# Kernel optimization log

Measured on AMD Instinct MI355X. Metric: run time of the kernel, lower is better.

The kernel has to match this reference:

```python
import jax, jax.numpy as jnp
import numpy as np

B, T, C = 2, 2048, 2048
H = 16
HS = C // H           # 128
ROT = HS // 2         # 64 partial-rotary dims
BASE = 10000.0


def setup_inputs() -> dict:
    key = jax.random.key(0)
    ks = jax.random.split(key, 9)
    s = 1.0 / np.sqrt(C)
    return {
        "x": jax.random.normal(ks[0], (B, T, C), jnp.float32),
        "Wq": jax.random.normal(ks[1], (C, C), jnp.float32) * s,
        "bq": jax.random.normal(ks[2], (C,), jnp.float32) * 0.02,
        "Wk": jax.random.normal(ks[3], (C, C), jnp.float32) * s,
        "bk": jax.random.normal(ks[4], (C,), jnp.float32) * 0.02,
        "Wv": jax.random.normal(ks[5], (C, C), jnp.float32) * s,
        "bv": jax.random.normal(ks[6], (C,), jnp.float32) * 0.02,
        "Wo": jax.random.normal(ks[7], (C, C), jnp.float32) * s,
        "bo": jax.random.normal(ks[8], (C,), jnp.float32) * 0.02,
    }


def _rotate_half(u):
    u1, u2 = u[..., : u.shape[-1] // 2], u[..., u.shape[-1] // 2 :]
    return jnp.concatenate((-u2, u1), axis=-1)


def _rope_tables(t_len):
    inv_freq = 1.0 / (BASE ** (jnp.arange(0, ROT, 2, dtype=jnp.float32) / ROT))
    freqs = jnp.arange(t_len, dtype=jnp.float32)[:, None] * inv_freq[None, :]
    emb = jnp.concatenate((freqs, freqs), axis=-1)  # [T, ROT]
    return jnp.cos(emb), jnp.sin(emb)


def reference(x, Wq, bq, Wk, bk, Wv, bv, Wo, bo):
    Bs, Ts, Cs = x.shape
    q = (x @ Wq.T + bq).reshape(Bs, Ts, H, HS).transpose(0, 2, 1, 3)  # [B,H,T,HS]
    k = (x @ Wk.T + bk).reshape(Bs, Ts, H, HS).transpose(0, 2, 1, 3)
    v = (x @ Wv.T + bv).reshape(Bs, Ts, H, HS).transpose(0, 2, 1, 3)

    # partial rotary on first ROT dims of each head
    cos, sin = _rope_tables(Ts)  # [T, ROT] broadcast over B,H
    q_rot, q_pass = q[..., :ROT], q[..., ROT:]
    k_rot, k_pass = k[..., :ROT], k[..., ROT:]
    q_rot = q_rot * cos + _rotate_half(q_rot) * sin
    k_rot = k_rot * cos + _rotate_half(k_rot) * sin
    q = jnp.concatenate((q_rot, q_pass), axis=-1)
    k = jnp.concatenate((k_rot, k_pass), axis=-1)

    att = jnp.einsum("bhqd,bhkd->bhqk", q, k) * (1.0 / np.sqrt(HS))
    causal = jnp.tril(jnp.ones((Ts, Ts), dtype=bool))
    att = jnp.where(causal, att, jnp.float32(-jnp.inf))
    att = jax.nn.softmax(att, axis=-1)
    out = jnp.einsum("bhqk,bhkd->bhqd", att, v)          # [B,H,T,HS]
    out = out.transpose(0, 2, 1, 3).reshape(Bs, Ts, Cs)  # [B,T,C]
    return out @ Wo.T + bo
```

## Files before the change

### kernel.cpp

```cpp
#include <hip/hip_runtime.h>
#include <hip/hip_bf16.h>

#define Bdim 2
#define Tdim 2048
#define Cdim 2048
#define Hn   16

using bf16x8 = __attribute__((ext_vector_type(8))) short;
using f32x4  = __attribute__((ext_vector_type(4))) float;
using f32x16 = __attribute__((ext_vector_type(16))) float;
typedef __hip_bfloat16 bf16;

#define VMWAIT(n) asm volatile("s_waitcnt vmcnt(" #n ")" ::: "memory")
#define CROW(r, hi) (((r) & 3) + 8 * ((r) >> 2) + 4 * (hi))
#define QS2 ((float)(0.08838834764831845 * 1.4426950408889634))
#define THR2 11.5415603f

__device__ __forceinline__ void load_lds16(const void* g, void* l) {
  __builtin_amdgcn_global_load_lds(
      (const __attribute__((address_space(1))) void*)g,
      (__attribute__((address_space(3))) void*)l, 16, 0, 0);
}

__device__ __forceinline__ float bf2f(unsigned short u) {
  union { unsigned int i; float f; } x; x.i = ((unsigned int)u) << 16; return x.f;
}
__device__ __forceinline__ unsigned short f2bf(float f) {
  bf16 h = __float2bfloat16(f); return *(unsigned short*)&h;
}
__device__ __forceinline__ unsigned cvtpk(float lo, float hi) {
  unsigned r;
  asm volatile("v_cvt_pk_bf16_f32 %0, %1, %2" : "=v"(r) : "v"(lo), "v"(hi));
  return r;
}

__global__ __launch_bounds__(256) void cvt_all(const float* __restrict__ x,
                                               const float* __restrict__ w0,
                                               const float* __restrict__ w1,
                                               const float* __restrict__ w2,
                                               const float* __restrict__ w3,
                                               bf16* __restrict__ dx,
                                               bf16* __restrict__ d0,
                                               bf16* __restrict__ d1,
                                               bf16* __restrict__ d2,
                                               bf16* __restrict__ d3) {
  const int NX = (Bdim * Tdim * Cdim) / 4;
  const int NW = (Cdim * Cdim) / 4;
  int i = blockIdx.x * 256 + threadIdx.x;
  int stride = gridDim.x * 256;
  for (; i < NX + 4 * NW; i += stride) {
    const float* s; bf16* d; int j;
    if (i < NX) { s = x; d = dx; j = i; }
    else {
      int k = i - NX;
      int wsel = k >> 20;
      j = k & (NW - 1);
      s = wsel == 0 ? w0 : wsel == 1 ? w1 : wsel == 2 ? w2 : w3;
      d = wsel == 0 ? d0 : wsel == 1 ? d1 : wsel == 2 ? d2 : d3;
    }
    float4 v = ((const float4*)s)[j];
    ushort4 o;
    o.x = f2bf(v.x); o.y = f2bf(v.y); o.z = f2bf(v.z); o.w = f2bf(v.w);
    ((ushort4*)d)[j] = o;
  }
}

__global__ __launch_bounds__(256) void rope_tables_k(float2* __restrict__ cst) {
  int idx = blockIdx.x * blockDim.x + threadIdx.x;
  if (idx >= Tdim * 32) return;
  int t = idx >> 5, i = idx & 31;
  double f = pow(10000.0, -(double)i / 32.0);
  double ang = (double)t * f;
  cst[idx] = make_float2((float)cos(ang), (float)sin(ang));
}

__global__ __launch_bounds__(512, 2) void gemmQKV(
    const bf16* __restrict__ A, const bf16* __restrict__ Wcat,
    const float* __restrict__ b0, const float* __restrict__ b1, const float* __restrict__ b2,
    bf16* __restrict__ oq, bf16* __restrict__ ok, bf16* __restrict__ vt,
    const float2* __restrict__ cst) {
  extern __shared__ char lds[];
  const int K = 2048;
  const int tid = threadIdx.x, lane = tid & 63, wid = tid >> 6;
  const int l15 = lane & 15, lhi = lane >> 4;
  const int wr = wid >> 2, wc = wid & 3;

  const int q8 = gridDim.x >> 3;
  const int swz = ((int)blockIdx.x & 7) * q8 + ((int)blockIdx.x >> 3);
  const int bm = (swz >> 4) * 128;
  const int strip = swz & 15;

  const int rA = tid >> 3;
  const int sl = tid & 7;
  const bf16* thrA = A + (size_t)(bm + rA) * K + ((sl ^ (rA & 7)) << 3);
  const int colB = strip * 384 + ((rA >> 5) * 96) + (rA & 31);
  const bf16* thrB = Wcat + (size_t)colB * K + ((sl ^ (rA & 7)) << 3);
  const int wbase = wid * 1024;

#define BUF(T) (lds + (((T) & 1) ? 65536 : 0))
#define SAU(T, U) load_lds16(thrA + (size_t)(U) * 64 * 2048 + (T) * 64, \
                             BUF(T) + (U) * 8192 + wbase)
#define SBU(T, NT, U) load_lds16(thrB + (size_t)((NT) * 32 + (U) * 192) * 2048 + (T) * 64, \
                                 BUF(T) + 16384 + (NT) * 16384 + (U) * 8192 + wbase)

  f32x4 acc[4][6] = {};
  const int NT = 32;
  const int asw = (l15 & 7) << 4;
  bf16x8 afr[4][2], bfr[2][2];

#define READA(T)                                                                 \
  _Pragma("unroll")                                                              \
  for (int mi = 0; mi < 4; ++mi)                                                 \
    _Pragma("unroll")                                                            \
    for (int kk = 0; kk < 2; ++kk)                                               \
      afr[mi][kk] = *(const bf16x8*)(BUF(T) + (wr * 64 + mi * 16 + l15) * 128    \
                                     + ((kk * 64 + lhi * 16) ^ asw));

#define READB(T, NT_)                                                            \
  _Pragma("unroll")                                                              \
  for (int j = 0; j < 2; ++j)                                                    \
    _Pragma("unroll")                                                            \
    for (int kk = 0; kk < 2; ++kk)                                               \
      bfr[j][kk] = *(const bf16x8*)(BUF(T) + 16384 + (NT_) * 16384               \
                                    + (wc * 32 + j * 16 + l15) * 128             \
                                    + ((kk * 64 + lhi * 16) ^ asw));

#define MF(NT_)                                                                  \
  __builtin_amdgcn_s_setprio(1);                                                 \
  _Pragma("unroll")                                                              \
  for (int mi = 0; mi < 4; ++mi)                                                 \
    _Pragma("unroll")                                                            \
    for (int j = 0; j < 2; ++j)                                                  \
      _Pragma("unroll")                                                          \
      for (int kk = 0; kk < 2; ++kk)                                             \
        acc[mi][(NT_) * 2 + j] = __builtin_amdgcn_mfma_f32_16x16x32_bf16(        \
            afr[mi][kk], bfr[j][kk], acc[mi][(NT_) * 2 + j], 0, 0, 0);           \
  __builtin_amdgcn_s_setprio(0);

#define BARS()                                                                   \
  __builtin_amdgcn_s_barrier();                                                  \
  asm volatile("s_waitcnt lgkmcnt(0)" ::: "memory");                             \
  __builtin_amdgcn_sched_barrier(0);

#define BARE() __builtin_amdgcn_s_barrier();

  SAU(0, 0); SAU(0, 1);
  SBU(0, 0, 0); SBU(0, 0, 1);
  SBU(0, 1, 0); SBU(0, 1, 1);
  SBU(0, 2, 0); SBU(0, 2, 1);
  SAU(1, 0); SAU(1, 1);
  SBU(1, 0, 0); SBU(1, 0, 1);
  SBU(1, 1, 0); SBU(1, 1, 1);
  VMWAIT(6);
  __builtin_amdgcn_s_barrier();

  for (int t = 0; t < NT - 2; ++t) {
    READA(t); READB(t, 0);
    SBU(t + 1, 2, 0); SBU(t + 1, 2, 1);
    BARS(); MF(0); BARE();
    READB(t, 1);
    SAU(t + 2, 0); SAU(t + 2, 1);
    SBU(t + 2, 0, 0); SBU(t + 2, 0, 1);
    BARS(); MF(1); BARE();
    READB(t, 2);
    SBU(t + 2, 1, 0); SBU(t + 2, 1, 1);
    VMWAIT(6);
    BARS(); MF(2); BARE();
  }
  {
    const int t = NT - 2;
    READA(t); READB(t, 0);
    SBU(t + 1, 2, 0); SBU(t + 1, 2, 1);
    BARS(); MF(0); BARE();
    READB(t, 1);
    BARS(); MF(1); BARE();
    READB(t, 2);
    VMWAIT(0);
    BARS(); MF(2); BARE();
  }
  {
    const int t = NT - 1;
    READA(t); READB(t, 0);
    BARS(); MF(0); BARE();
    READB(t, 1);
    BARS(); MF(1); BARE();
    READB(t, 2);
    BARS(); MF(2); BARE();
  }

  __syncthreads();
  if (wc == 3) {
    #pragma unroll
    for (int mi = 0; mi < 4; ++mi)
      #pragma unroll
      for (int j = 0; j < 2; ++j) {
        const int col = strip * 384 + 288 + j * 16 + l15;
        const int mat = col >> 11;
        const float bv = (mat == 0 ? b0 : mat == 1 ? b1 : b2)[col & 2047];
        f32x4 v = acc[mi][j];
        v[0] += bv; v[1] += bv; v[2] += bv; v[3] += bv;
        *(f32x4*)(lds + ((((wr * 4 + mi) * 2 + j) * 4 + lhi) * 16 + l15) * 16) = v;
      }
  }
  __syncthreads();

  #pragma unroll
  for (int mi = 0; mi < 4; ++mi) {
    const int row = bm + wr * 64 + mi * 16 + lhi * 4;
    const int bb = row >> 11, tt = row & 2047;
    #pragma unroll
    for (int nt = 0; nt < 3; ++nt)
      #pragma unroll
      for (int j = 0; j < 2; ++j) {
        const int col = strip * 384 + wc * 96 + nt * 32 + j * 16 + l15;
        const int mat = col >> 11;
        const int ocol = col & 2047;
        const float bv = (mat == 0 ? b0 : mat == 1 ? b1 : b2)[ocol];
        if (mat == 2) {
          const int hh = ocol >> 7, dd = ocol & 127;
          ushort4 pk;
          pk.x = f2bf(acc[mi][nt * 2 + j][0] + bv);
          pk.y = f2bf(acc[mi][nt * 2 + j][1] + bv);
          pk.z = f2bf(acc[mi][nt * 2 + j][2] + bv);
          pk.w = f2bf(acc[mi][nt * 2 + j][3] + bv);
          *(ushort4*)(vt + ((size_t)((bb * 16 + hh) * 128 + dd)) * 2048 + tt) = pk;
        } else {
          const float qs = (mat == 0) ? QS2 : 1.0f;
          bf16* obf = (mat == 0) ? oq : ok;
          int cat;
          if (wc == 0)      cat = (nt == 0) ? 1 : (nt == 1) ? 2 : 0;
          else if (wc == 1) cat = (nt == 1) ? 1 : (nt == 2) ? 2 : 0;
          else if (wc == 2) cat = (nt == 2) ? 3 : 0;
          else              cat = (nt == 0) ? 2 : 0;
          if (cat == 0) {
            #pragma unroll
            for (int r = 0; r < 4; ++r)
              obf[(size_t)(row + r) * 2048 + ocol] =
                  __float2bfloat16((acc[mi][nt * 2 + j][r] + bv) * qs);
          } else if (cat == 1) {
            const float bv1 = (mat == 0 ? b0 : b1)[ocol + 32];
            const int d = j * 16 + l15;
            #pragma unroll
            for (int r = 0; r < 4; ++r) {
              float2 cs = cst[(tt + r) * 32 + d];
              float u0 = acc[mi][nt * 2 + j][r] + bv;
              float u1 = acc[mi][(nt + 1) * 2 + j][r] + bv1;
              obf[(size_t)(row + r) * 2048 + ocol] =
                  __float2bfloat16((u0 * cs.x - u1 * cs.y) * qs);
              obf[(size_t)(row + r) * 2048 + ocol + 32] =
                  __float2bfloat16((u1 * cs.x + u0 * cs.y) * qs);
            }
          } else if (cat == 3) {
            f32x4 ux = *(const f32x4*)(lds + ((((wr * 4 + mi) * 2 + j) * 4 + lhi) * 16 + l15) * 16);
            const int d = j * 16 + l15;
            #pragma unroll
            for (int r = 0; r < 4; ++r) {
              float2 cs = cst[(tt + r) * 32 + d];
              float u0 = acc[mi][4 + j][r] + bv;
              float u1 = ux[r];
              obf[(size_t)(row + r) * 2048 + ocol] =
                  __float2bfloat16((u0 * cs.x - u1 * cs.y) * qs);
              obf[(size_t)(row + r) * 2048 + ocol + 32] =
                  __float2bfloat16((u1 * cs.x + u0 * cs.y) * qs);
            }
          }
        }
      }
  }
#undef BUF
#undef SAU
#undef SBU
#undef READA
#undef READB
#undef MF
#undef BARS
#undef BARE
}

__global__ __launch_bounds__(512, 2) void gemmWo(
    const bf16* __restrict__ A, const bf16* __restrict__ W0,
    const float* __restrict__ b0, float* __restrict__ out, int K, int nby) {
  extern __shared__ char lds[];
  const int tid = threadIdx.x, lane = tid & 63, wid = tid >> 6;
  const int l15 = lane & 15, lhi = lane >> 4;
  const int wr = wid >> 2, wc = wid & 3;
  const int fb = (wc & 1) | ((wc >> 1) << 2);

  const int q8 = gridDim.x >> 3;
  const int swz = ((int)blockIdx.x & 7) * q8 + ((int)blockIdx.x >> 3);
  const int bm = (swz / nby) * 128, bn = (swz % nby) * 256;
  const bf16* Asrc = A + (size_t)bm * K;
  const bf16* Wsrc = W0 + (size_t)bn * K;

  const bf16 *sA0, *sA1, *sB00, *sB01, *sB10, *sB11;
  {
    int c = tid, r = c >> 3, sl = c & 7;
    size_t off = (size_t)r * K + ((sl ^ (r & 7)) << 3);
    sA0 = Asrc + off;
    sA1 = Asrc + (size_t)64 * K + off;
    sB00 = Wsrc + off;
    sB10 = Wsrc + (size_t)128 * K + off;
  }
  {
    int c = 512 + tid, r = c >> 3, sl = c & 7;
    size_t off = (size_t)r * K + ((sl ^ (r & 7)) << 3);
    sB01 = Wsrc + off;
    sB11 = Wsrc + (size_t)128 * K + off;
  }
  const int ldsA = wid * 1024;

#define SA0(t) load_lds16(sA0 + (t) * 64, lds + ((t) & 1) * 49152 + ldsA)
#define SA1(t) load_lds16(sA1 + (t) * 64, lds + ((t) & 1) * 49152 + 8192 + ldsA)
#define SB0(t) { load_lds16(sB00 + (t) * 64, lds + ((t) & 1) * 49152 + 16384 + ldsA); \
                 load_lds16(sB01 + (t) * 64, lds + ((t) & 1) * 49152 + 24576 + ldsA); }
#define SB1(t) { load_lds16(sB10 + (t) * 64, lds + ((t) & 1) * 49152 + 32768 + ldsA); \
                 load_lds16(sB11 + (t) * 64, lds + ((t) & 1) * 49152 + 40960 + ldsA); }

  f32x4 acc[4][4] = {};
  const int NT = K / 64;
  const int NI = NT / 2;
  const int asw = (l15 & 7) << 4;
  bf16x8 afr[2][2], bfr0[2][2], bfr1[2][2];

#define READ_A(BASE)                                                            \
  _Pragma("unroll")                                                             \
  for (int ii = 0; ii < 2; ++ii)                                                \
    _Pragma("unroll")                                                           \
    for (int kk = 0; kk < 2; ++kk)                                              \
      afr[ii][kk] = *(const bf16x8*)((BASE) + (wr * 32 + ii * 16 + l15) * 128   \
                                     + ((kk * 64 + lhi * 16) ^ asw));

#define READ_B(BASE, DST)                                                       \
  _Pragma("unroll")                                                             \
  for (int j = 0; j < 2; ++j)                                                   \
    _Pragma("unroll")                                                           \
    for (int kk = 0; kk < 2; ++kk)                                              \
      DST[j][kk] = *(const bf16x8*)((BASE) + ((fb + 2 * j) * 16 + l15) * 128    \
                                    + ((kk * 64 + lhi * 16) ^ asw));

#define MFMA_Q(MH, NH, BF)                                                      \
  __builtin_amdgcn_s_setprio(1);                                                \
  _Pragma("unroll")                                                             \
  for (int ii = 0; ii < 2; ++ii)                                                \
    _Pragma("unroll")                                                           \
    for (int j = 0; j < 2; ++j)                                                 \
      _Pragma("unroll")                                                         \
      for (int kk = 0; kk < 2; ++kk)                                            \
        acc[(MH) * 2 + ii][(NH) * 2 + j] =                                      \
            __builtin_amdgcn_mfma_f32_16x16x32_bf16(                            \
                afr[ii][kk], BF[j][kk], acc[(MH) * 2 + ii][(NH) * 2 + j], 0, 0, 0); \
  __builtin_amdgcn_s_setprio(0);

#define BAR_IN()                                                                \
  __builtin_amdgcn_s_barrier();                                                 \
  asm volatile("s_waitcnt lgkmcnt(0)" ::: "memory");                            \
  __builtin_amdgcn_sched_barrier(0);

#define BAR_OUT() __builtin_amdgcn_s_barrier();

  SA0(0); SB0(0); SB1(0); SA1(0);
  SA0(1); SB0(1); SB1(1);
  VMWAIT(5);
  __builtin_amdgcn_s_barrier();

  char* const buf0 = lds;
  char* const buf1 = lds + 49152;

  for (int i = 0; i < NI; ++i) {
    const int t0 = 2 * i, t1 = t0 + 1;
    const bool lastI = (i == NI - 1);

    READ_A(buf0);
    READ_B(buf0 + 16384, bfr0);
    SA1(t1);
    BAR_IN(); MFMA_Q(0, 0, bfr0); BAR_OUT();

    READ_B(buf0 + 32768, bfr1);
    if (!lastI) SA0(t0 + 2);
    BAR_IN(); MFMA_Q(0, 1, bfr1); BAR_OUT();

    READ_A(buf0 + 8192);
    if (!lastI) SB0(t0 + 2);
    BAR_IN(); MFMA_Q(1, 0, bfr0); BAR_OUT();

    if (!lastI) { SB1(t0 + 2); VMWAIT(5); } else VMWAIT(0);
    BAR_IN(); MFMA_Q(1, 1, bfr1); BAR_OUT();

    READ_A(buf1);
    READ_B(buf1 + 16384, bfr0);
    if (!lastI) SA1(t0 + 2);
    BAR_IN(); MFMA_Q(0, 0, bfr0); BAR_OUT();

    READ_B(buf1 + 32768, bfr1);
    if (!lastI) SA0(t1 + 2);
    BAR_IN(); MFMA_Q(0, 1, bfr1); BAR_OUT();

    READ_A(buf1 + 8192);
    if (!lastI) SB0(t1 + 2);
    BAR_IN(); MFMA_Q(1, 0, bfr0); BAR_OUT();

    if (!lastI) { SB1(t1 + 2); VMWAIT(5); }
    BAR_IN(); MFMA_Q(1, 1, bfr1); BAR_OUT();
  }

  #pragma unroll
  for (int mi = 0; mi < 4; ++mi) {
    const int row = bm + (mi >> 1) * 64 + wr * 32 + (mi & 1) * 16 + lhi * 4;
    #pragma unroll
    for (int nj = 0; nj < 4; ++nj) {
      const int col = bn + (nj >> 1) * 128 + (fb + 2 * (nj & 1)) * 16 + l15;
      const float bv = b0[col];
      #pragma unroll
      for (int r = 0; r < 4; ++r)
        out[(size_t)(row + r) * 2048 + col] = acc[mi][nj][r] + bv;
    }
  }
#undef SA0
#undef SA1
#undef SB0
#undef SB1
#undef READ_A
#undef READ_B
#undef MFMA_Q
#undef BAR_IN
#undef BAR_OUT
}

__global__ __launch_bounds__(256, 2) void attn_kernel(const bf16* __restrict__ Q,
                                                      const bf16* __restrict__ Kb,
                                                      const bf16* __restrict__ Vt,
                                                      bf16* __restrict__ O) {
  extern __shared__ char lds[];
  const int tid = threadIdx.x, lane = tid & 63, wave = tid >> 6;
  const int l31 = lane & 31, hi = lane >> 5;
  const int hi16 = hi << 4;

  const int bid = blockIdx.x;
  const int half = bid >> 8;
  const int idx = bid & 255;
  const int g = idx >> 5;
  const int qt = half ? g : (15 - g);
  const int bh = idx & 31;
  const int b = bh >> 4, h = bh & 15;
  const size_t bT = (size_t)b * Tdim;

  const int qb = qt * 128 + wave * 32;
  const int myq = qb + l31;

  bf16x8 qf[8];
  {
    const bf16* qrow = Q + (bT + myq) * Cdim + h * 128;
    #pragma unroll
    for (int ds = 0; ds < 8; ++ds)
      qf[ds] = *(const bf16x8*)(qrow + ds * 16 + hi * 8);
  }

  auto stageKV = [&](int kt) {
    const int k0 = kt * 64;
    char* kb = lds + (kt & 1) * 16384;
    char* vb = lds + 32768 + (kt & 1) * 16384;
    #pragma unroll
    for (int i = 0; i < 4; ++i) {
      int cb = i * 256 + wave * 64;
      int c = cb + lane;
      {
        int row = c >> 4, slot = c & 15;
        load_lds16(Kb + (bT + k0 + row) * Cdim + h * 128 + ((slot ^ (row & 7)) << 3),
                   kb + cb * 16);
      }
      {
        int row = c >> 3, slot = c & 7;
        load_lds16(Vt + ((size_t)(bh * 128 + row)) * Tdim + k0 + ((slot ^ (row & 7)) << 3),
                   vb + cb * 16);
      }
    }
  };

  f32x16 o[4] = {};
  float mrun = -1e30f, lrun = 0.f;

  const int nt = 2 * (qt + 1);
  stageKV(0);

  for (int kt = 0; kt < nt; ++kt) {
    if (kt + 1 < nt) { stageKV(kt + 1); VMWAIT(8); } else { VMWAIT(0); }
    __syncthreads();
    const char* kbuf = lds + (kt & 1) * 16384;
    const char* vbuf = lds + 32768 + (kt & 1) * 16384;
    const int k0 = kt * 64;

    const bool active = (k0 <= qb + 31);
    if (active) {
      f32x16 s0 = {}, s1 = {};
      const int krow0 = l31, krow1 = 32 + l31;
      const int ksw = (l31 & 7) << 4;
      __builtin_amdgcn_s_setprio(1);
      #pragma unroll
      for (int ds = 0; ds < 8; ++ds) {
        const int boff = (ds * 32 + hi16) ^ ksw;
        bf16x8 kf0 = *(const bf16x8*)(kbuf + krow0 * 256 + boff);
        bf16x8 kf1 = *(const bf16x8*)(kbuf + krow1 * 256 + boff);
        s0 = __builtin_amdgcn_mfma_f32_32x32x16_bf16(kf0, qf[ds], s0, 0, 0, 0);
        s1 = __builtin_amdgcn_mfma_f32_32x32x16_bf16(kf1, qf[ds], s1, 0, 0, 0);
      }
      __builtin_amdgcn_s_setprio(0);

      if (k0 + 63 > qb) {
        #pragma unroll
        for (int r = 0; r < 16; ++r) {
          const int key = k0 + CROW(r, hi);
          if (key > myq)      s0[r] = -1e30f;
          if (key + 32 > myq) s1[r] = -1e30f;
        }
      }

      float mx = s0[0];
      #pragma unroll
      for (int r = 1; r < 16; ++r) mx = fmaxf(mx, s0[r]);
      #pragma unroll
      for (int r = 0; r < 16; ++r) mx = fmaxf(mx, s1[r]);
      mx = fmaxf(mx, __shfl_xor(mx, 32));
      if (!__all(mx <= mrun + THR2)) {
        const float mnew = fmaxf(mrun, mx);
        const float scl = __builtin_amdgcn_exp2f(mrun - mnew);
        lrun *= scl;
        #pragma unroll
        for (int r = 0; r < 16; ++r) {
          const float sr = __shfl(scl, CROW(r, hi));
          o[0][r] *= sr; o[1][r] *= sr; o[2][r] *= sr; o[3][r] *= sr;
        }
        mrun = mnew;
      }
      float p0[16], p1[16];
      float ps = 0.f;
      #pragma unroll
      for (int r = 0; r < 16; ++r) {
        p0[r] = __builtin_amdgcn_exp2f(s0[r] - mrun); ps += p0[r];
        p1[r] = __builtin_amdgcn_exp2f(s1[r] - mrun); ps += p1[r];
      }
      ps += __shfl_xor(ps, 32);
      lrun += ps;

      unsigned u0[8], u1[8];
      #pragma unroll
      for (int gg = 0; gg < 4; ++gg) {
        u0[gg * 2 + 0] = cvtpk(p0[gg * 4 + 0], p0[gg * 4 + 1]);
        u0[gg * 2 + 1] = cvtpk(p0[gg * 4 + 2], p0[gg * 4 + 3]);
        u1[gg * 2 + 0] = cvtpk(p1[gg * 4 + 0], p1[gg * 4 + 1]);
        u1[gg * 2 + 1] = cvtpk(p1[gg * 4 + 2], p1[gg * 4 + 3]);
      }
      bf16x8 paf[4];
      #pragma unroll
      for (int s = 0; s < 2; ++s) {
        const unsigned* us = s ? u1 : u0;
        #pragma unroll
        for (int gp = 0; gp < 2; ++gp) {
          unsigned snd0 = hi ? us[4 * gp + 0] : us[4 * gp + 2];
          unsigned snd1 = hi ? us[4 * gp + 1] : us[4 * gp + 3];
          unsigned rcv0 = __shfl_xor((int)snd0, 32);
          unsigned rcv1 = __shfl_xor((int)snd1, 32);
          union { unsigned w[4]; bf16x8 v; } fr;
          if (hi == 0) {
            fr.w[0] = us[4 * gp + 0]; fr.w[1] = us[4 * gp + 1];
            fr.w[2] = rcv0;           fr.w[3] = rcv1;
          } else {
            fr.w[0] = rcv0;           fr.w[1] = rcv1;
            fr.w[2] = us[4 * gp + 2]; fr.w[3] = us[4 * gp + 3];
          }
          paf[s * 2 + gp] = fr.v;
        }
      }

      __builtin_amdgcn_s_setprio(1);
      #pragma unroll
      for (int dblk = 0; dblk < 4; ++dblk) {
        const int d = dblk * 32 + l31;
        const int vswz = (d & 7) << 4;
        #pragma unroll
        for (int ks = 0; ks < 4; ++ks) {
          bf16x8 vf = *(const bf16x8*)(vbuf + d * 128 + ((ks * 32 + hi16) ^ vswz));
          o[dblk] = __builtin_amdgcn_mfma_f32_32x32x16_bf16(paf[ks], vf, o[dblk], 0, 0, 0);
        }
      }
      __builtin_amdgcn_s_setprio(0);
    }
    __syncthreads();
  }

  const float inv = 1.f / lrun;
  #pragma unroll
  for (int r = 0; r < 16; ++r) {
    const float ir = __shfl(inv, CROW(r, hi));
    const int qrow = qb + CROW(r, hi);
    bf16* orow = O + (bT + qrow) * Cdim + h * 128;
    #pragma unroll
    for (int dblk = 0; dblk < 4; ++dblk)
      orow[dblk * 32 + l31] = __float2bfloat16(o[dblk][r] * ir);
  }
}

extern "C" void kernel_launch(void* const* d_in, const int* in_sizes, int n_in,
                              void* d_out, int out_size, void* d_ws, size_t ws_size,
                              hipStream_t stream) {
  const float* x  = (const float*)d_in[0];
  const float* Wq = (const float*)d_in[1];
  const float* bq = (const float*)d_in[2];
  const float* Wk = (const float*)d_in[3];
  const float* bk = (const float*)d_in[4];
  const float* Wv = (const float*)d_in[5];
  const float* bv = (const float*)d_in[6];
  const float* Wo = (const float*)d_in[7];
  const float* bo = (const float*)d_in[8];

  char* ws = (char*)d_ws;
  const size_t SZ_X  = (size_t)Bdim * Tdim * Cdim * 2;
  const size_t SZ_W  = (size_t)Cdim * Cdim * 2;
  bf16* x_bf  = (bf16*)(ws);
  bf16* Wq_bf = (bf16*)(ws + SZ_X);
  bf16* Wk_bf = (bf16*)(ws + SZ_X + SZ_W);
  bf16* Wv_bf = (bf16*)(ws + SZ_X + 2 * SZ_W);
  bf16* Wo_bf = (bf16*)(ws + SZ_X + 3 * SZ_W);
  bf16* q_bf  = (bf16*)(ws + SZ_X + 4 * SZ_W);
  bf16* k_bf  = (bf16*)(ws + 2 * SZ_X + 4 * SZ_W);
  bf16* v_t   = (bf16*)(ws + 3 * SZ_X + 4 * SZ_W);
  bf16* a_bf  = (bf16*)(ws + 4 * SZ_X + 4 * SZ_W);
  float2* cst = (float2*)(ws + 5 * SZ_X + 4 * SZ_W);

  const int K = Cdim;

  rope_tables_k<<<(Tdim * 32 + 255) / 256, 256, 0, stream>>>(cst);
  cvt_all<<<2048, 256, 0, stream>>>(x, Wq, Wk, Wv, Wo,
                                    x_bf, Wq_bf, Wk_bf, Wv_bf, Wo_bf);

  gemmQKV<<<512, 512, 131072, stream>>>(
      x_bf, Wq_bf, bq, bk, bv, q_bf, k_bf, v_t, cst);

  attn_kernel<<<512, 256, 65536, stream>>>(q_bf, k_bf, v_t, a_bf);

  gemmWo<<<256, 512, 98304, stream>>>(
      a_bf, Wo_bf, bo, (float*)d_out, K, 8);
}
```

Measured before the change: 236.3 us.

## Restructure QKV GEMM to 256x384 tiles with 32x32 MFMA and triple-buffered K=32 stages

The fused QKV projection kernel now uses 256-row by 384-column block tiles (256 blocks instead of 512) with 32x32x16 bf16 MFMA instructions in place of 16x16x32. Each K step is 32 wide, and three LDS stage buffers are rotated so global-to-LDS loads run two steps ahead. The epilogue is rewritten for the 32x32 accumulator layout and still applies RoPE, scaling and the V transpose. The aim is more data reuse per block and fewer LDS reads per MFMA. The cost is only 256 blocks, which may leave the grid with fewer waves than there are CUs to fill, and a reduced occupancy margin.

```diff
diff --git a/kernel.cpp b/kernel.cpp
--- a/kernel.cpp
+++ b/kernel.cpp
@@ -80,199 +80,195 @@
     bf16* __restrict__ oq, bf16* __restrict__ ok, bf16* __restrict__ vt,
     const float2* __restrict__ cst) {
   extern __shared__ char lds[];
-  const int K = 2048;
   const int tid = threadIdx.x, lane = tid & 63, wid = tid >> 6;
-  const int l15 = lane & 15, lhi = lane >> 4;
+  const int l31 = lane & 31, hi = lane >> 5;
   const int wr = wid >> 2, wc = wid & 3;
+  const int wbase = wid * 1024;
 
   const int q8 = gridDim.x >> 3;
   const int swz = ((int)blockIdx.x & 7) * q8 + ((int)blockIdx.x >> 3);
-  const int bm = (swz >> 4) * 128;
+  const int bm = (swz >> 4) * 256;
   const int strip = swz & 15;
 
-  const int rA = tid >> 3;
-  const int sl = tid & 7;
-  const bf16* thrA = A + (size_t)(bm + rA) * K + ((sl ^ (rA & 7)) << 3);
-  const int colB = strip * 384 + ((rA >> 5) * 96) + (rA & 31);
-  const bf16* thrB = Wcat + (size_t)colB * K + ((sl ^ (rA & 7)) << 3);
-  const int wbase = wid * 1024;
-
-#define BUF(T) (lds + (((T) & 1) ? 65536 : 0))
-#define SAU(T, U) load_lds16(thrA + (size_t)(U) * 64 * 2048 + (T) * 64, \
-                             BUF(T) + (U) * 8192 + wbase)
-#define SBU(T, NT, U) load_lds16(thrB + (size_t)((NT) * 32 + (U) * 192) * 2048 + (T) * 64, \
-                                 BUF(T) + 16384 + (NT) * 16384 + (U) * 8192 + wbase)
-
-  f32x4 acc[4][6] = {};
-  const int NT = 32;
-  const int asw = (l15 & 7) << 4;
-  bf16x8 afr[4][2], bfr[2][2];
-
-#define READA(T)                                                                 \
-  _Pragma("unroll")                                                              \
-  for (int mi = 0; mi < 4; ++mi)                                                 \
-    _Pragma("unroll")                                                            \
-    for (int kk = 0; kk < 2; ++kk)                                               \
-      afr[mi][kk] = *(const bf16x8*)(BUF(T) + (wr * 64 + mi * 16 + l15) * 128    \
-                                     + ((kk * 64 + lhi * 16) ^ asw));
-
-#define READB(T, NT_)                                                            \
-  _Pragma("unroll")                                                              \
-  for (int j = 0; j < 2; ++j)                                                    \
-    _Pragma("unroll")                                                            \
-    for (int kk = 0; kk < 2; ++kk)                                               \
-      bfr[j][kk] = *(const bf16x8*)(BUF(T) + 16384 + (NT_) * 16384               \
-                                    + (wc * 32 + j * 16 + l15) * 128             \
-                                    + ((kk * 64 + lhi * 16) ^ asw));
-
-#define MF(NT_)                                                                  \
-  __builtin_amdgcn_s_setprio(1);                                                 \
-  _Pragma("unroll")                                                              \
-  for (int mi = 0; mi < 4; ++mi)                                                 \
-    _Pragma("unroll")                                                            \
-    for (int j = 0; j < 2; ++j)                                                  \
-      _Pragma("unroll")                                                          \
-      for (int kk = 0; kk < 2; ++kk)                                             \
-        acc[mi][(NT_) * 2 + j] = __builtin_amdgcn_mfma_f32_16x16x32_bf16(        \
-            afr[mi][kk], bfr[j][kk], acc[mi][(NT_) * 2 + j], 0, 0, 0);           \
+  const int rS = tid >> 2, sS = tid & 3;
+  const int ssw = (sS ^ ((rS >> 1) & 3)) << 3;
+  const bf16* thrA = A + (size_t)(bm + rS) * 2048 + ssw;
+  const bf16* thrB = Wcat + (size_t)(strip * 384 + rS) * 2048 + ssw;
+
+#define SA(T, DB) { load_lds16(thrA + (T) * 32, (DB) + wbase);                              \
+                    load_lds16(thrA + (size_t)128 * 2048 + (T) * 32, (DB) + 8192 + wbase); }
+#define SB(T, DB) { load_lds16(thrB + (T) * 32, (DB) + 16384 + wbase);                      \
+                    load_lds16(thrB + (size_t)128 * 2048 + (T) * 32, (DB) + 24576 + wbase); \
+                    load_lds16(thrB + (size_t)256 * 2048 + (T) * 32, (DB) + 32768 + wbase); }
+
+  f32x16 acc[4][3] = {};
+  bf16x8 afr[4], bfr[3];
+  const int q2 = (l31 >> 1) & 3;
+  const int aoff = (wr * 128 + l31) * 64;
+  const int boff = 16384 + (wc * 96 + l31) * 64;
+  const int sl0 = (hi ^ q2) << 4;
+  const int sl1 = sl0 ^ 32;
+
+#define READF(PB, SL)                                                        \
+  {                                                                          \
+    const char* _p = (PB);                                                   \
+    _Pragma("unroll")                                                        \
+    for (int m_ = 0; m_ < 4; ++m_)                                           \
+      afr[m_] = *(const bf16x8*)(_p + aoff + m_ * 2048 + (SL));              \
+    _Pragma("unroll")                                                        \
+    for (int n_ = 0; n_ < 3; ++n_)                                           \
+      bfr[n_] = *(const bf16x8*)(_p + boff + n_ * 2048 + (SL));              \
+  }
+
+#define MF12()                                                               \
+  __builtin_amdgcn_s_setprio(1);                                             \
+  _Pragma("unroll")                                                          \
+  for (int m_ = 0; m_ < 4; ++m_)                                             \
+    _Pragma("unroll")                                                        \
+    for (int n_ = 0; n_ < 3; ++n_)                                           \
+      acc[m_][n_] = __builtin_amdgcn_mfma_f32_32x32x16_bf16(                 \
+          afr[m_], bfr[n_], acc[m_][n_], 0, 0, 0);                           \
   __builtin_amdgcn_s_setprio(0);
 
-#define BARS()                                                                   \
-  __builtin_amdgcn_s_barrier();                                                  \
-  asm volatile("s_waitcnt lgkmcnt(0)" ::: "memory");                             \
+#define BARS()                                                               \
+  __builtin_amdgcn_s_barrier();                                              \
+  asm volatile("s_waitcnt lgkmcnt(0)" ::: "memory");                         \
   __builtin_amdgcn_sched_barrier(0);
 
 #define BARE() __builtin_amdgcn_s_barrier();
 
-  SAU(0, 0); SAU(0, 1);
-  SBU(0, 0, 0); SBU(0, 0, 1);
-  SBU(0, 1, 0); SBU(0, 1, 1);
-  SBU(0, 2, 0); SBU(0, 2, 1);
-  SAU(1, 0); SAU(1, 1);
-  SBU(1, 0, 0); SBU(1, 0, 1);
-  SBU(1, 1, 0); SBU(1, 1, 1);
-  VMWAIT(6);
+  SA(0, lds); SB(0, lds);
+  SA(1, lds + 40960); SB(1, lds + 40960);
+  VMWAIT(5);
   __builtin_amdgcn_s_barrier();
 
+  const char* rb = lds;
+  char* sb = lds + 81920;
+  const int NT = 64;
+
   for (int t = 0; t < NT - 2; ++t) {
-    READA(t); READB(t, 0);
-    SBU(t + 1, 2, 0); SBU(t + 1, 2, 1);
-    BARS(); MF(0); BARE();
-    READB(t, 1);
-    SAU(t + 2, 0); SAU(t + 2, 1);
-    SBU(t + 2, 0, 0); SBU(t + 2, 0, 1);
-    BARS(); MF(1); BARE();
-    READB(t, 2);
-    SBU(t + 2, 1, 0); SBU(t + 2, 1, 1);
-    VMWAIT(6);
-    BARS(); MF(2); BARE();
+    READF(rb, sl0);
+    SA(t + 2, sb);
+    BARS(); MF12(); BARE();
+    READF(rb, sl1);
+    SB(t + 2, sb);
+    VMWAIT(5);
+    BARS(); MF12(); BARE();
+    rb = (rb == lds + 81920) ? lds : rb + 40960;
+    sb = (sb == lds + 81920) ? lds : sb + 40960;
   }
   {
-    const int t = NT - 2;
-    READA(t); READB(t, 0);
-    SBU(t + 1, 2, 0); SBU(t + 1, 2, 1);
-    BARS(); MF(0); BARE();
-    READB(t, 1);
-    BARS(); MF(1); BARE();
-    READB(t, 2);
+    READF(rb, sl0);
+    BARS(); MF12(); BARE();
+    READF(rb, sl1);
     VMWAIT(0);
-    BARS(); MF(2); BARE();
+    BARS(); MF12(); BARE();
+    rb = (rb == lds + 81920) ? lds : rb + 40960;
   }
   {
-    const int t = NT - 1;
-    READA(t); READB(t, 0);
-    BARS(); MF(0); BARE();
-    READB(t, 1);
-    BARS(); MF(1); BARE();
-    READB(t, 2);
-    BARS(); MF(2); BARE();
+    READF(rb, sl0);
+    BARS(); MF12(); BARE();
+    READF(rb, sl1);
+    BARS(); MF12(); BARE();
   }
 
   __syncthreads();
   if (wc == 3) {
+    const int col0 = strip * 384 + 288;
+    const int mat = col0 >> 11;
+    if (mat < 2) {
+      const int oc0 = col0 & 2047;
+      const float bv = (mat == 0 ? b0 : b1)[oc0 + l31];
+      #pragma unroll
+      for (int m = 0; m < 4; ++m)
+        #pragma unroll
+        for (int g = 0; g < 4; ++g) {
+          f32x4 v;
+          v[0] = acc[m][0][4 * g + 0] + bv;
+          v[1] = acc[m][0][4 * g + 1] + bv;
+          v[2] = acc[m][0][4 * g + 2] + bv;
+          v[3] = acc[m][0][4 * g + 3] + bv;
+          *(f32x4*)(lds + (((((wr * 4 + m) * 4 + g) * 2 + hi) * 32) + l31) * 16) = v;
+        }
+    }
+  }
+  __syncthreads();
+
+  #pragma unroll
+  for (int m = 0; m < 4; ++m) {
+    const int rowb = bm + wr * 128 + m * 32;
+    const int bb = rowb >> 11, tb = rowb & 2047;
     #pragma unroll
-    for (int mi = 0; mi < 4; ++mi)
-      #pragma unroll
-      for (int j = 0; j < 2; ++j) {
-        const int col = strip * 384 + 288 + j * 16 + l15;
-        const int mat = col >> 11;
-        const float bv = (mat == 0 ? b0 : mat == 1 ? b1 : b2)[col & 2047];
-        f32x4 v = acc[mi][j];
-        v[0] += bv; v[1] += bv; v[2] += bv; v[3] += bv;
-        *(f32x4*)(lds + ((((wr * 4 + mi) * 2 + j) * 4 + lhi) * 16 + l15) * 16) = v;
-      }
-  }
-  __syncthreads();
-
-  #pragma unroll
-  for (int mi = 0; mi < 4; ++mi) {
-    const int row = bm + wr * 64 + mi * 16 + lhi * 4;
-    const int bb = row >> 11, tt = row & 2047;
-    #pragma unroll
-    for (int nt = 0; nt < 3; ++nt)
-      #pragma unroll
-      for (int j = 0; j < 2; ++j) {
-        const int col = strip * 384 + wc * 96 + nt * 32 + j * 16 + l15;
-        const int mat = col >> 11;
-        const int ocol = col & 2047;
-        const float bv = (mat == 0 ? b0 : mat == 1 ? b1 : b2)[ocol];
-        if (mat == 2) {
-          const int hh = ocol >> 7, dd = ocol & 127;
+    for (int n = 0; n < 3; ++n) {
+      const int col0 = strip * 384 + wc * 96 + n * 32;
+      const int mat = col0 >> 11;
+      const int oc0 = col0 & 2047;
+      const float bv = (mat == 0 ? b0 : mat == 1 ? b1 : b2)[oc0 + l31];
+      if (mat == 2) {
+        const int hh = oc0 >> 7;
+        bf16* dst = vt + ((size_t)((bb * 16 + hh) * 128 + (oc0 & 127) + l31)) * 2048 + tb;
+        #pragma unroll
+        for (int g = 0; g < 4; ++g) {
           ushort4 pk;
-          pk.x = f2bf(acc[mi][nt * 2 + j][0] + bv);
-          pk.y = f2bf(acc[mi][nt * 2 + j][1] + bv);
-          pk.z = f2bf(acc[mi][nt * 2 + j][2] + bv);
-          pk.w = f2bf(acc[mi][nt * 2 + j][3] + bv);
-          *(ushort4*)(vt + ((size_t)((bb * 16 + hh) * 128 + dd)) * 2048 + tt) = pk;
-        } else {
-          const float qs = (mat == 0) ? QS2 : 1.0f;
-          bf16* obf = (mat == 0) ? oq : ok;
-          int cat;
-          if (wc == 0)      cat = (nt == 0) ? 1 : (nt == 1) ? 2 : 0;
-          else if (wc == 1) cat = (nt == 1) ? 1 : (nt == 2) ? 2 : 0;
-          else if (wc == 2) cat = (nt == 2) ? 3 : 0;
-          else              cat = (nt == 0) ? 2 : 0;
-          if (cat == 0) {
+          pk.x = f2bf(acc[m][n][4 * g + 0] + bv);
+          pk.y = f2bf(acc[m][n][4 * g + 1] + bv);
+          pk.z = f2bf(acc[m][n][4 * g + 2] + bv);
+          pk.w = f2bf(acc[m][n][4 * g + 3] + bv);
+          *(ushort4*)(dst + g * 8 + hi * 4) = pk;
+        }
+      } else {
+        const float qs = (mat == 0) ? QS2 : 1.0f;
+        bf16* obf = (mat == 0) ? oq : ok;
+        const int hb = (wc * 3 + n) & 3;
+        if (hb == 0) {
+          if (wc == 2 && n == 2) {
             #pragma unroll
-            for (int r = 0; r < 4; ++r)
-              obf[(size_t)(row + r) * 2048 + ocol] =
-                  __float2bfloat16((acc[mi][nt * 2 + j][r] + bv) * qs);
-          } else if (cat == 1) {
-            const float bv1 = (mat == 0 ? b0 : b1)[ocol + 32];
-            const int d = j * 16 + l15;
+            for (int g = 0; g < 4; ++g) {
+              f32x4 ux = *(const f32x4*)(lds + (((((wr * 4 + m) * 4 + g) * 2 + hi) * 32) + l31) * 16);
+              #pragma unroll
+              for (int j = 0; j < 4; ++j) {
+                const int r = 4 * g + j;
+                const int row = rowb + j + 8 * g + 4 * hi;
+                const int tt = row & 2047;
+                float2 cs = cst[tt * 32 + l31];
+                float u0 = acc[m][n][r] + bv;
+                float u1 = ux[j];
+                obf[(size_t)row * 2048 + oc0 + l31] =
+                    __float2bfloat16((u0 * cs.x - u1 * cs.y) * qs);
+                obf[(size_t)row * 2048 + oc0 + 32 + l31] =
+                    __float2bfloat16((u1 * cs.x + u0 * cs.y) * qs);
+              }
+            }
+          } else {
+            const float bv1 = (mat == 0 ? b0 : b1)[oc0 + 32 + l31];
             #pragma unroll
-            for (int r = 0; r < 4; ++r) {
-              float2 cs = cst[(tt + r) * 32 + d];
-              float u0 = acc[mi][nt * 2 + j][r] + bv;
-              float u1 = acc[mi][(nt + 1) * 2 + j][r] + bv1;
-              obf[(size_t)(row + r) * 2048 + ocol] =
+            for (int r = 0; r < 16; ++r) {
+              const int row = rowb + (r & 3) + 8 * (r >> 2) + 4 * hi;
+              const int tt = row & 2047;
+              float2 cs = cst[tt * 32 + l31];
+              float u0 = acc[m][n][r] + bv;
+              float u1 = acc[m][n + 1][r] + bv1;
+              obf[(size_t)row * 2048 + oc0 + l31] =
                   __float2bfloat16((u0 * cs.x - u1 * cs.y) * qs);
-              obf[(size_t)(row + r) * 2048 + ocol + 32] =
-                  __float2bfloat16((u1 * cs.x + u0 * cs.y) * qs);
-            }
-          } else if (cat == 3) {
-            f32x4 ux = *(const f32x4*)(lds + ((((wr * 4 + mi) * 2 + j) * 4 + lhi) * 16 + l15) * 16);
-            const int d = j * 16 + l15;
-            #pragma unroll
-            for (int r = 0; r < 4; ++r) {
-              float2 cs = cst[(tt + r) * 32 + d];
-              float u0 = acc[mi][4 + j][r] + bv;
-              float u1 = ux[r];
-              obf[(size_t)(row + r) * 2048 + ocol] =
-                  __float2bfloat16((u0 * cs.x - u1 * cs.y) * qs);
-              obf[(size_t)(row + r) * 2048 + ocol + 32] =
+              obf[(size_t)row * 2048 + oc0 + 32 + l31] =
                   __float2bfloat16((u1 * cs.x + u0 * cs.y) * qs);
             }
           }
+        } else if (hb >= 2) {
+          #pragma unroll
+          for (int r = 0; r < 16; ++r) {
+            const int row = rowb + (r & 3) + 8 * (r >> 2) + 4 * hi;
+            obf[(size_t)row * 2048 + oc0 + l31] =
+                __float2bfloat16((acc[m][n][r] + bv) * qs);
+          }
         }
       }
-  }
-#undef BUF
-#undef SAU
-#undef SBU
-#undef READA
-#undef READB
-#undef MF
+    }
+  }
+#undef SA
+#undef SB
+#undef READF
+#undef MF12
 #undef BARS
 #undef BARE
 }
@@ -632,7 +628,7 @@
   cvt_all<<<2048, 256, 0, stream>>>(x, Wq, Wk, Wv, Wo,
                                     x_bf, Wq_bf, Wk_bf, Wv_bf, Wo_bf);
 
-  gemmQKV<<<512, 512, 131072, stream>>>(
+  gemmQKV<<<256, 512, 122880, stream>>>(
       x_bf, Wq_bf, bq, bk, bv, q_bf, k_bf, v_t, cst);
 
   attn_kernel<<<512, 256, 65536, stream>>>(q_bf, k_bf, v_t, a_bf);
```

New measurement: 231.0 us. 2.2% less time.

## Retile QKV GEMM to 128x256 tiles reusing Wo GEMM pipeline with head-aligned rope epilogue

Applied to the files above, without the earlier changes.

Replaces the 128x384 QKV GEMM tile with a 128x256 tile structured like the Wo GEMM: quarter-tile MFMA phases, double-buffered 48KB LDS, and a column mapping (fb) so each wave holds both rotary halves of a head. The grid grows from 512 to 768 blocks with less LDS per block. The rope epilogue no longer needs an LDS exchange across waves. The intent is better occupancy and load balance and a simpler epilogue. The smaller N tile means less reuse of each A tile, at the cost of more global traffic.

```diff
diff --git a/kernel.cpp b/kernel.cpp
--- a/kernel.cpp
+++ b/kernel.cpp
@@ -84,197 +84,193 @@
   const int tid = threadIdx.x, lane = tid & 63, wid = tid >> 6;
   const int l15 = lane & 15, lhi = lane >> 4;
   const int wr = wid >> 2, wc = wid & 3;
+  const int fb = (wc & 1) | ((wc >> 1) << 2);
 
   const int q8 = gridDim.x >> 3;
   const int swz = ((int)blockIdx.x & 7) * q8 + ((int)blockIdx.x >> 3);
-  const int bm = (swz >> 4) * 128;
-  const int strip = swz & 15;
-
-  const int rA = tid >> 3;
-  const int sl = tid & 7;
-  const bf16* thrA = A + (size_t)(bm + rA) * K + ((sl ^ (rA & 7)) << 3);
-  const int colB = strip * 384 + ((rA >> 5) * 96) + (rA & 31);
-  const bf16* thrB = Wcat + (size_t)colB * K + ((sl ^ (rA & 7)) << 3);
-  const int wbase = wid * 1024;
-
-#define BUF(T) (lds + (((T) & 1) ? 65536 : 0))
-#define SAU(T, U) load_lds16(thrA + (size_t)(U) * 64 * 2048 + (T) * 64, \
-                             BUF(T) + (U) * 8192 + wbase)
-#define SBU(T, NT, U) load_lds16(thrB + (size_t)((NT) * 32 + (U) * 192) * 2048 + (T) * 64, \
-                                 BUF(T) + 16384 + (NT) * 16384 + (U) * 8192 + wbase)
-
-  f32x4 acc[4][6] = {};
-  const int NT = 32;
+  const int bm = (swz / 24) * 128;
+  const int strip = swz % 24;
+  const int mat = strip >> 3;
+  const bf16* Asrc = A + (size_t)bm * K;
+  const bf16* Wsrc = Wcat + (size_t)(strip * 256) * K;
+
+  const bf16 *sA0, *sA1, *sB00, *sB01, *sB10, *sB11;
+  {
+    int c = tid, r = c >> 3, sl = c & 7;
+    size_t off = (size_t)r * K + ((sl ^ (r & 7)) << 3);
+    sA0 = Asrc + off;
+    sA1 = Asrc + (size_t)64 * K + off;
+    sB00 = Wsrc + off;
+    sB10 = Wsrc + (size_t)128 * K + off;
+  }
+  {
+    int c = 512 + tid, r = c >> 3, sl = c & 7;
+    size_t off = (size_t)r * K + ((sl ^ (r & 7)) << 3);
+    sB01 = Wsrc + off;
+    sB11 = Wsrc + (size_t)128 * K + off;
+  }
+  const int ldsA = wid * 1024;
+
+#define SA0(t) load_lds16(sA0 + (t) * 64, lds + ((t) & 1) * 49152 + ldsA)
+#define SA1(t) load_lds16(sA1 + (t) * 64, lds + ((t) & 1) * 49152 + 8192 + ldsA)
+#define SB0(t) { load_lds16(sB00 + (t) * 64, lds + ((t) & 1) * 49152 + 16384 + ldsA); \
+                 load_lds16(sB01 + (t) * 64, lds + ((t) & 1) * 49152 + 24576 + ldsA); }
+#define SB1(t) { load_lds16(sB10 + (t) * 64, lds + ((t) & 1) * 49152 + 32768 + ldsA); \
+                 load_lds16(sB11 + (t) * 64, lds + ((t) & 1) * 49152 + 40960 + ldsA); }
+
+  f32x4 acc[4][4] = {};
+  const int NT = K / 64;
+  const int NI = NT / 2;
   const int asw = (l15 & 7) << 4;
-  bf16x8 afr[4][2], bfr[2][2];
-
-#define READA(T)                                                                 \
-  _Pragma("unroll")                                                              \
-  for (int mi = 0; mi < 4; ++mi)                                                 \
-    _Pragma("unroll")                                                            \
-    for (int kk = 0; kk < 2; ++kk)                                               \
-      afr[mi][kk] = *(const bf16x8*)(BUF(T) + (wr * 64 + mi * 16 + l15) * 128    \
+  bf16x8 afr[2][2], bfr0[2][2], bfr1[2][2];
+
+#define READ_A(BASE)                                                            \
+  _Pragma("unroll")                                                             \
+  for (int ii = 0; ii < 2; ++ii)                                                \
+    _Pragma("unroll")                                                           \
+    for (int kk = 0; kk < 2; ++kk)                                              \
+      afr[ii][kk] = *(const bf16x8*)((BASE) + (wr * 32 + ii * 16 + l15) * 128   \
                                      + ((kk * 64 + lhi * 16) ^ asw));
 
-#define READB(T, NT_)                                                            \
-  _Pragma("unroll")                                                              \
-  for (int j = 0; j < 2; ++j)                                                    \
-    _Pragma("unroll")                                                            \
-    for (int kk = 0; kk < 2; ++kk)                                               \
-      bfr[j][kk] = *(const bf16x8*)(BUF(T) + 16384 + (NT_) * 16384               \
-                                    + (wc * 32 + j * 16 + l15) * 128             \
+#define READ_B(BASE, DST)                                                       \
+  _Pragma("unroll")                                                             \
+  for (int j = 0; j < 2; ++j)                                                   \
+    _Pragma("unroll")                                                           \
+    for (int kk = 0; kk < 2; ++kk)                                              \
+      DST[j][kk] = *(const bf16x8*)((BASE) + ((fb + 2 * j) * 16 + l15) * 128    \
                                     + ((kk * 64 + lhi * 16) ^ asw));
 
-#define MF(NT_)                                                                  \
-  __builtin_amdgcn_s_setprio(1);                                                 \
-  _Pragma("unroll")                                                              \
-  for (int mi = 0; mi < 4; ++mi)                                                 \
-    _Pragma("unroll")                                                            \
-    for (int j = 0; j < 2; ++j)                                                  \
-      _Pragma("unroll")                                                          \
-      for (int kk = 0; kk < 2; ++kk)                                             \
-        acc[mi][(NT_) * 2 + j] = __builtin_amdgcn_mfma_f32_16x16x32_bf16(        \
-            afr[mi][kk], bfr[j][kk], acc[mi][(NT_) * 2 + j], 0, 0, 0);           \
+#define MFMA_Q(MH, NH, BF)                                                      \
+  __builtin_amdgcn_s_setprio(1);                                                \
+  _Pragma("unroll")                                                             \
+  for (int ii = 0; ii < 2; ++ii)                                                \
+    _Pragma("unroll")                                                           \
+    for (int j = 0; j < 2; ++j)                                                 \
+      _Pragma("unroll")                                                         \
+      for (int kk = 0; kk < 2; ++kk)                                            \
+        acc[(MH) * 2 + ii][(NH) * 2 + j] =                                      \
+            __builtin_amdgcn_mfma_f32_16x16x32_bf16(                            \
+                afr[ii][kk], BF[j][kk], acc[(MH) * 2 + ii][(NH) * 2 + j], 0, 0, 0); \
   __builtin_amdgcn_s_setprio(0);
 
-#define BARS()                                                                   \
-  __builtin_amdgcn_s_barrier();                                                  \
-  asm volatile("s_waitcnt lgkmcnt(0)" ::: "memory");                             \
+#define BAR_IN()                                                                \
+  __builtin_amdgcn_s_barrier();                                                 \
+  asm volatile("s_waitcnt lgkmcnt(0)" ::: "memory");                            \
   __builtin_amdgcn_sched_barrier(0);
 
-#define BARE() __builtin_amdgcn_s_barrier();
-
-  SAU(0, 0); SAU(0, 1);
-  SBU(0, 0, 0); SBU(0, 0, 1);
-  SBU(0, 1, 0); SBU(0, 1, 1);
-  SBU(0, 2, 0); SBU(0, 2, 1);
-  SAU(1, 0); SAU(1, 1);
-  SBU(1, 0, 0); SBU(1, 0, 1);
-  SBU(1, 1, 0); SBU(1, 1, 1);
-  VMWAIT(6);
+#define BAR_OUT() __builtin_amdgcn_s_barrier();
+
+  SA0(0); SB0(0); SB1(0); SA1(0);
+  SA0(1); SB0(1); SB1(1);
+  VMWAIT(5);
   __builtin_amdgcn_s_barrier();
 
-  for (int t = 0; t < NT - 2; ++t) {
-    READA(t); READB(t, 0);
-    SBU(t + 1, 2, 0); SBU(t + 1, 2, 1);
-    BARS(); MF(0); BARE();
-    READB(t, 1);
-    SAU(t + 2, 0); SAU(t + 2, 1);
-    SBU(t + 2, 0, 0); SBU(t + 2, 0, 1);
-    BARS(); MF(1); BARE();
-    READB(t, 2);
-    SBU(t + 2, 1, 0); SBU(t + 2, 1, 1);
-    VMWAIT(6);
-    BARS(); MF(2); BARE();
-  }
-  {
-    const int t = NT - 2;
-    READA(t); READB(t, 0);
-    SBU(t + 1, 2, 0); SBU(t + 1, 2, 1);
-    BARS(); MF(0); BARE();
-    READB(t, 1);
-    BARS(); MF(1); BARE();
-    READB(t, 2);
-    VMWAIT(0);
-    BARS(); MF(2); BARE();
-  }
-  {
-    const int t = NT - 1;
-    READA(t); READB(t, 0);
-    BARS(); MF(0); BARE();
-    READB(t, 1);
-    BARS(); MF(1); BARE();
-    READB(t, 2);
-    BARS(); MF(2); BARE();
-  }
-
-  __syncthreads();
-  if (wc == 3) {
-    #pragma unroll
-    for (int mi = 0; mi < 4; ++mi)
-      #pragma unroll
-      for (int j = 0; j < 2; ++j) {
-        const int col = strip * 384 + 288 + j * 16 + l15;
-        const int mat = col >> 11;
-        const float bv = (mat == 0 ? b0 : mat == 1 ? b1 : b2)[col & 2047];
-        f32x4 v = acc[mi][j];
-        v[0] += bv; v[1] += bv; v[2] += bv; v[3] += bv;
-        *(f32x4*)(lds + ((((wr * 4 + mi) * 2 + j) * 4 + lhi) * 16 + l15) * 16) = v;
-      }
-  }
-  __syncthreads();
-
+  char* const buf0 = lds;
+  char* const buf1 = lds + 49152;
+
+  for (int i = 0; i < NI; ++i) {
+    const int t0 = 2 * i, t1 = t0 + 1;
+    const bool lastI = (i == NI - 1);
+
+    READ_A(buf0);
+    READ_B(buf0 + 16384, bfr0);
+    SA1(t1);
+    BAR_IN(); MFMA_Q(0, 0, bfr0); BAR_OUT();
+
+    READ_B(buf0 + 32768, bfr1);
+    if (!lastI) SA0(t0 + 2);
+    BAR_IN(); MFMA_Q(0, 1, bfr1); BAR_OUT();
+
+    READ_A(buf0 + 8192);
+    if (!lastI) SB0(t0 + 2);
+    BAR_IN(); MFMA_Q(1, 0, bfr0); BAR_OUT();
+
+    if (!lastI) { SB1(t0 + 2); VMWAIT(5); } else VMWAIT(0);
+    BAR_IN(); MFMA_Q(1, 1, bfr1); BAR_OUT();
+
+    READ_A(buf1);
+    READ_B(buf1 + 16384, bfr0);
+    if (!lastI) SA1(t0 + 2);
+    BAR_IN(); MFMA_Q(0, 0, bfr0); BAR_OUT();
+
+    READ_B(buf1 + 32768, bfr1);
+    if (!lastI) SA0(t1 + 2);
+    BAR_IN(); MFMA_Q(0, 1, bfr1); BAR_OUT();
+
+    READ_A(buf1 + 8192);
+    if (!lastI) SB0(t1 + 2);
+    BAR_IN(); MFMA_Q(1, 0, bfr0); BAR_OUT();
+
+    if (!lastI) { SB1(t1 + 2); VMWAIT(5); }
+    BAR_IN(); MFMA_Q(1, 1, bfr1); BAR_OUT();
+  }
+
+  const int ocb = (strip & 7) * 256;
   #pragma unroll
   for (int mi = 0; mi < 4; ++mi) {
-    const int row = bm + wr * 64 + mi * 16 + lhi * 4;
-    const int bb = row >> 11, tt = row & 2047;
+    const int row0 = bm + (mi >> 1) * 64 + wr * 32 + (mi & 1) * 16 + lhi * 4;
+    const int bb = row0 >> 11, tb = row0 & 2047;
     #pragma unroll
-    for (int nt = 0; nt < 3; ++nt)
-      #pragma unroll
-      for (int j = 0; j < 2; ++j) {
-        const int col = strip * 384 + wc * 96 + nt * 32 + j * 16 + l15;
-        const int mat = col >> 11;
-        const int ocol = col & 2047;
-        const float bv = (mat == 0 ? b0 : mat == 1 ? b1 : b2)[ocol];
-        if (mat == 2) {
-          const int hh = ocol >> 7, dd = ocol & 127;
+    for (int nh = 0; nh < 2; ++nh) {
+      const int chead = ocb + nh * 128;
+      if (mat == 2) {
+        #pragma unroll
+        for (int j = 0; j < 2; ++j) {
+          const int col = chead + (fb + 2 * j) * 16 + l15;
+          const int hh = col >> 7, dd = col & 127;
+          const float bv = b2[col];
           ushort4 pk;
-          pk.x = f2bf(acc[mi][nt * 2 + j][0] + bv);
-          pk.y = f2bf(acc[mi][nt * 2 + j][1] + bv);
-          pk.z = f2bf(acc[mi][nt * 2 + j][2] + bv);
-          pk.w = f2bf(acc[mi][nt * 2 + j][3] + bv);
-          *(ushort4*)(vt + ((size_t)((bb * 16 + hh) * 128 + dd)) * 2048 + tt) = pk;
+          pk.x = f2bf(acc[mi][nh * 2 + j][0] + bv);
+          pk.y = f2bf(acc[mi][nh * 2 + j][1] + bv);
+          pk.z = f2bf(acc[mi][nh * 2 + j][2] + bv);
+          pk.w = f2bf(acc[mi][nh * 2 + j][3] + bv);
+          *(ushort4*)(vt + ((size_t)((bb * 16 + hh) * 128 + dd)) * 2048 + tb) = pk;
+        }
+      } else {
+        const float qs = (mat == 0) ? QS2 : 1.0f;
+        bf16* obf = (mat == 0) ? oq : ok;
+        const float* bp = (mat == 0) ? b0 : b1;
+        if (wc < 2) {
+          const int collo = chead + fb * 16 + l15;
+          const int d = fb * 16 + l15;
+          const float bl = bp[collo], bh = bp[collo + 32];
+          #pragma unroll
+          for (int r = 0; r < 4; ++r) {
+            const int row = row0 + r;
+            const int tt = row & 2047;
+            float2 cs = cst[tt * 32 + d];
+            float u0 = acc[mi][nh * 2 + 0][r] + bl;
+            float u1 = acc[mi][nh * 2 + 1][r] + bh;
+            obf[(size_t)row * 2048 + collo] =
+                __float2bfloat16((u0 * cs.x - u1 * cs.y) * qs);
+            obf[(size_t)row * 2048 + collo + 32] =
+                __float2bfloat16((u1 * cs.x + u0 * cs.y) * qs);
+          }
         } else {
-          const float qs = (mat == 0) ? QS2 : 1.0f;
-          bf16* obf = (mat == 0) ? oq : ok;
-          int cat;
-          if (wc == 0)      cat = (nt == 0) ? 1 : (nt == 1) ? 2 : 0;
-          else if (wc == 1) cat = (nt == 1) ? 1 : (nt == 2) ? 2 : 0;
-          else if (wc == 2) cat = (nt == 2) ? 3 : 0;
-          else              cat = (nt == 0) ? 2 : 0;
-          if (cat == 0) {
-            #pragma unroll
-            for (int r = 0; r < 4; ++r)
-              obf[(size_t)(row + r) * 2048 + ocol] =
-                  __float2bfloat16((acc[mi][nt * 2 + j][r] + bv) * qs);
-          } else if (cat == 1) {
-            const float bv1 = (mat == 0 ? b0 : b1)[ocol + 32];
-            const int d = j * 16 + l15;
+          #pragma unroll
+          for (int j = 0; j < 2; ++j) {
+            const int col = chead + (fb + 2 * j) * 16 + l15;
+            const float bv = bp[col];
             #pragma unroll
             for (int r = 0; r < 4; ++r) {
-              float2 cs = cst[(tt + r) * 32 + d];
-              float u0 = acc[mi][nt * 2 + j][r] + bv;
-              float u1 = acc[mi][(nt + 1) * 2 + j][r] + bv1;
-              obf[(size_t)(row + r) * 2048 + ocol] =
-                  __float2bfloat16((u0 * cs.x - u1 * cs.y) * qs);
-              obf[(size_t)(row + r) * 2048 + ocol + 32] =
-                  __float2bfloat16((u1 * cs.x + u0 * cs.y) * qs);
-            }
-          } else if (cat == 3) {
-            f32x4 ux = *(const f32x4*)(lds + ((((wr * 4 + mi) * 2 + j) * 4 + lhi) * 16 + l15) * 16);
-            const int d = j * 16 + l15;
-            #pragma unroll
-            for (int r = 0; r < 4; ++r) {
-              float2 cs = cst[(tt + r) * 32 + d];
-              float u0 = acc[mi][4 + j][r] + bv;
-              float u1 = ux[r];
-              obf[(size_t)(row + r) * 2048 + ocol] =
-                  __float2bfloat16((u0 * cs.x - u1 * cs.y) * qs);
-              obf[(size_t)(row + r) * 2048 + ocol + 32] =
-                  __float2bfloat16((u1 * cs.x + u0 * cs.y) * qs);
+              const int row = row0 + r;
+              obf[(size_t)row * 2048 + col] =
+                  __float2bfloat16((acc[mi][nh * 2 + j][r] + bv) * qs);
             }
           }
         }
       }
-  }
-#undef BUF
-#undef SAU
-#undef SBU
-#undef READA
-#undef READB
-#undef MF
-#undef BARS
-#undef BARE
+    }
+  }
+#undef SA0
+#undef SA1
+#undef SB0
+#undef SB1
+#undef READ_A
+#undef READ_B
+#undef MFMA_Q
+#undef BAR_IN
+#undef BAR_OUT
 }
 
 __global__ __launch_bounds__(512, 2) void gemmWo(
@@ -632,7 +628,7 @@
   cvt_all<<<2048, 256, 0, stream>>>(x, Wq, Wk, Wv, Wo,
                                     x_bf, Wq_bf, Wk_bf, Wv_bf, Wo_bf);
 
-  gemmQKV<<<512, 512, 131072, stream>>>(
+  gemmQKV<<<768, 512, 98304, stream>>>(
       x_bf, Wq_bf, bq, bk, bv, q_bf, k_bf, v_t, cst);
 
   attn_kernel<<<512, 256, 65536, stream>>>(q_bf, k_bf, v_t, a_bf);
```

New measurement: 244.6 us. +3.5%, slower.
